# Kernel tuning notes

Measured on AMD Instinct MI355X. Metric: run time of the kernel, lower is better.

## Reference

```python
import jax, jax.numpy as jnp
import numpy as np

N_EVENTS = 16384   # original pixel events
D = 128            # input_size
H = 128            # hidden_size
K = 9              # kernel 3x3 -> patch coords
S = 2048           # number of patch sequences
LMAX = 108         # max sequence length
T = 147456         # total patch events = sum(lengths) = 9 * N_EVENTS


def setup_inputs() -> dict:
    key = jax.random.key(0)
    ks = jax.random.split(key, 8)
    events = jax.random.normal(ks[0], (N_EVENTS, D), jnp.float32)
    pos_id = jax.random.randint(ks[1], (T,), 0, K, dtype=jnp.int32)
    orig_event_idx = jax.random.randint(ks[2], (T,), 0, N_EVENTS, dtype=jnp.int32)
    # alternating 36/108 lengths: 1024*36 + 1024*108 = 147456 = T
    lengths = jnp.where(jnp.arange(S) % 2 == 0, 36, 108).astype(jnp.int32)
    std = float(np.sqrt(2.0 / (D + H)))
    scatter_w = jax.random.normal(ks[3], (K, H, D), jnp.float32) * std
    gather_w = jax.random.normal(ks[4], (K, H, H), jnp.float32) * std
    lstm_std = float(1.0 / np.sqrt(H))
    w_ih = jax.random.uniform(ks[5], (4 * H, H), jnp.float32, -lstm_std, lstm_std)
    w_hh = jax.random.uniform(ks[6], (4 * H, H), jnp.float32, -lstm_std, lstm_std)
    ln_g = jnp.ones((H,), jnp.float32)
    ln_b = jnp.zeros((H,), jnp.float32)
    return dict(events=events, scatter_w=scatter_w, gather_w=gather_w,
                w_ih=w_ih, w_hh=w_hh, ln_g=ln_g, ln_b=ln_b,
                pos_id=pos_id, orig_event_idx=orig_event_idx, lengths=lengths)


def _pos_proj(x, W, pos_id):
    # position-indexed projection: out[t] = W[pos_id[t]] @ x[t]
    # loop over small fixed K=9 with masked accumulate (matches the torch loop)
    out = jnp.zeros((x.shape[0], W.shape[1]), x.dtype)
    for k in range(W.shape[0]):
        out = out + jnp.where((pos_id == k)[:, None], x @ W[k].T, 0.0)
    return out


def reference(events, scatter_w, gather_w, w_ih, w_hh, ln_g, ln_b,
              pos_id, orig_event_idx, lengths):
    # scatter events to patch replicas
    x = events[orig_event_idx]                           # [T, D]
    x = _pos_proj(x, scatter_w, pos_id)                  # [T, H]

    # flat (sequence-major) -> padded [S, LMAX, H]
    seq_offsets = jnp.cumsum(lengths) - lengths          # [S]
    seq_ids = jnp.repeat(jnp.arange(S), lengths, total_repeat_length=T)
    pos_in_seq = jnp.arange(T) - seq_offsets[seq_ids]
    padded = jnp.zeros((S, LMAX, H), x.dtype).at[seq_ids, pos_in_seq].set(x)

    # single-layer bias-free LSTM (pytorch gate order i, f, g, o), zero init.
    # zero-padding after each sequence's valid region leaves valid outputs
    # identical to a PackedSequence LSTM.
    def step(carry, xt):                                 # xt: [S, H]
        h, c = carry
        gates = xt @ w_ih.T + h @ w_hh.T                 # [S, 4H]
        i, f, g, o = jnp.split(gates, 4, axis=-1)
        c = jax.nn.sigmoid(f) * c + jax.nn.sigmoid(i) * jnp.tanh(g)
        h = jax.nn.sigmoid(o) * jnp.tanh(c)
        return (h, c), h

    init = (jnp.zeros((S, H), x.dtype), jnp.zeros((S, H), x.dtype))
    _, hs = jax.lax.scan(step, init, jnp.swapaxes(padded, 0, 1))  # [LMAX, S, H]
    o_flat = jnp.swapaxes(hs, 0, 1)[seq_ids, pos_in_seq]          # [T, H]

    o_flat = _pos_proj(o_flat, gather_w, pos_id)                  # [T, H]

    # gather patch events back to pixel events (scatter-add) + residual + LN
    out = jnp.zeros((N_EVENTS, H), x.dtype).at[orig_event_idx].add(o_flat)
    out = out + events                                   # input_proj is None (D == H)
    mu = jnp.mean(out, axis=-1, keepdims=True)
    var = jnp.var(out, axis=-1, keepdims=True)
    out = (out - mu) * jax.lax.rsqrt(var + 1e-5) * ln_g + ln_b
    return out
```

## Files before the change

### kernel.cpp

```cpp
#include <hip/hip_runtime.h>

#define N_EVENTS 16384
#define DIM 128
#define NK 9
#define NSEQ 2048
#define TT 147456
#define CHUNK 64
#define NCHUNK_MAX (TT/CHUNK + NK)
#define NHBLK 576

typedef __attribute__((ext_vector_type(8))) short bf16x8;
typedef __attribute__((ext_vector_type(4))) float f32x4;
typedef __attribute__((ext_vector_type(4))) int i32x4;

#define OFF_EV     0UL
#define OFF_WC     (OFF_EV   + (size_t)N_EVENTS*DIM*2)
#define OFF_SCAT   (OFF_WC   + (size_t)512*256*2)
#define OFF_GATH   (OFF_SCAT + (size_t)NK*DIM*DIM*2)
#define OFF_XS     (OFF_GATH + (size_t)NK*DIM*DIM*2)
#define OFF_HS     (OFF_XS   + (size_t)TT*DIM*2)
#define OFF_KLIST  (OFF_HS   + (size_t)TT*DIM*2)
#define OFF_ACC    (OFF_KLIST+ (size_t)TT*4)
#define OFF_SEQOFF (OFF_ACC  + (size_t)N_EVENTS*DIM*4)
#define OFF_GROUP  (OFF_SEQOFF + (size_t)NSEQ*4)
#define OFF_MISC   (OFF_GROUP  + (size_t)NSEQ*4)
#define OFF_BH     (OFF_MISC   + 256UL)

__device__ __forceinline__ short f2b(float f) {
    union { float f; unsigned u; } v; v.f = f;
    unsigned r = (v.u + 0x7FFFu + ((v.u >> 16) & 1u)) >> 16;
    return (short)r;
}

__device__ __forceinline__ float fsig(float x) {
    return __builtin_amdgcn_rcpf(1.f + __expf(-x));
}
__device__ __forceinline__ float ftanh(float x) {
    return 1.f - 2.f * __builtin_amdgcn_rcpf(__expf(2.f * x) + 1.f);
}

__global__ void convert_kernel(const float* __restrict__ ev, const float* __restrict__ wih,
                               const float* __restrict__ whh, const float* __restrict__ sw,
                               const float* __restrict__ gw,
                               short* __restrict__ evb, short* __restrict__ wcb,
                               short* __restrict__ swb, short* __restrict__ gwb,
                               float* __restrict__ acc) {
    int idx = blockIdx.x * blockDim.x + threadIdx.x;
    if (idx < N_EVENTS * DIM) { evb[idx] = f2b(ev[idx]); acc[idx] = 0.f; }
    if (idx < 512 * DIM) {
        int j = idx >> 7, d = idx & 127;
        wcb[j * 256 + d]       = f2b(wih[idx]);
        wcb[j * 256 + 128 + d] = f2b(whh[idx]);
    }
    if (idx < NK * DIM * DIM) { swb[idx] = f2b(sw[idx]); gwb[idx] = f2b(gw[idx]); }
}

__global__ void hist_kernel(const int* __restrict__ pos, int* __restrict__ blockhist) {
    __shared__ int h[NK];
    int tid = threadIdx.x;
    if (tid < NK) h[tid] = 0;
    __syncthreads();
    atomicAdd(&h[pos[blockIdx.x * 256 + tid]], 1);
    __syncthreads();
    if (tid < NK) blockhist[blockIdx.x * NK + tid] = h[tid];
}

__global__ void scan_kernel(int* __restrict__ blockhist, int* __restrict__ misc) {
    __shared__ int h[NHBLK * NK];
    int tid = threadIdx.x;
    for (int i = tid; i < NHBLK * NK; i += 256) h[i] = blockhist[i];
    __syncthreads();
    if (tid < NK) {
        int run = 0;
        for (int b = 0; b < NHBLK; b++) {
            int v = h[b * NK + tid];
            h[b * NK + tid] = run;
            run += v;
        }
        misc[tid] = run;
    }
    __syncthreads();
    if (tid == 0) {
        int ko = 0, co = 0;
        for (int k = 0; k < NK; k++) {
            int c = misc[k];
            misc[32 + k] = ko;
            misc[48 + k] = co;
            ko += c;
            co += (c + CHUNK - 1) / CHUNK;
        }
        misc[48 + NK] = co;
    }
    __syncthreads();
    for (int i = tid; i < NHBLK * NK; i += 256) blockhist[i] = h[i];
}

__global__ void setup_kernel(const int* __restrict__ lengths,
                             int* __restrict__ seq_off, int* __restrict__ grouped) {
    __shared__ int lens[NSEQ];
    __shared__ int tsum[256], tlong[256];
    int tid = threadIdx.x;
    for (int i = tid; i < NSEQ; i += 256) lens[i] = lengths[i];
    __syncthreads();
    int base = tid * 8;
    int ls[8]; int s = 0, lc = 0;
    #pragma unroll
    for (int i = 0; i < 8; i++) { ls[i] = lens[base + i]; s += ls[i]; lc += (ls[i] > 64) ? 1 : 0; }
    tsum[tid] = s; tlong[tid] = lc;
    __syncthreads();
    for (int d = 1; d < 256; d <<= 1) {
        int a = (tid >= d) ? tsum[tid - d] : 0;
        int b = (tid >= d) ? tlong[tid - d] : 0;
        __syncthreads();
        tsum[tid] += a; tlong[tid] += b;
        __syncthreads();
    }
    int nlong_total = tlong[255];
    int excl = tsum[tid] - s;
    int excl_long = tlong[tid] - lc;
    int run = 0, runl = 0;
    #pragma unroll
    for (int i = 0; i < 8; i++) {
        int sid = base + i;
        seq_off[sid] = excl + run;
        int longs_before = excl_long + runl;
        if (ls[i] > 64) { grouped[longs_before] = sid; runl++; }
        else            { grouped[nlong_total + (sid - longs_before)] = sid; }
        run += ls[i];
    }
}

__global__ void fill2_kernel(const int* __restrict__ pos, const int* __restrict__ blockhist,
                             const int* __restrict__ misc, int* __restrict__ klist) {
    __shared__ int off[NK];
    int tid = threadIdx.x;
    if (tid < NK) off[tid] = misc[32 + tid] + blockhist[blockIdx.x * NK + tid];
    __syncthreads();
    int t = blockIdx.x * 256 + tid;
    int p = atomicAdd(&off[pos[t]], 1);
    klist[p] = t;
}

__global__ void bucket_gemm(const short* __restrict__ src, const short* __restrict__ wall,
                            const int* __restrict__ klist, const int* __restrict__ misc,
                            const int* __restrict__ orig, short* __restrict__ xs_out,
                            float* __restrict__ acc, int mode) {
    const int* chunkoff = misc + 48;
    int b = blockIdx.x;
    if (b >= chunkoff[NK]) return;
    int k = 0;
    while (k < NK - 1 && chunkoff[k + 1] <= b) k++;
    int lc = b - chunkoff[k];
    int cnt = misc[k];
    int base = misc[32 + k] + lc * CHUNK;
    int nv = min(CHUNK, cnt - lc * CHUNK);

    __shared__ int tok[CHUNK], dst[CHUNK];
    __shared__ short A[CHUNK * 136];
    int tid = threadIdx.x;
    if (tid < CHUNK) {
        int tv = klist[base + ((tid < nv) ? tid : 0)];
        tok[tid] = tv;
        dst[tid] = orig[tv];
    }
    __syncthreads();
    {
        int row = tid >> 2, part = tid & 3;
        int ridx = (mode == 0) ? dst[row] : tok[row];
        const i32x4* s4 = (const i32x4*)(src + (size_t)ridx * DIM + part * 32);
        i32x4* d4 = (i32x4*)(A + row * 136 + part * 32);
        d4[0] = s4[0]; d4[1] = s4[1]; d4[2] = s4[2]; d4[3] = s4[3];
    }
    __syncthreads();
    int wave = tid >> 6, lane = tid & 63, l15 = lane & 15, q = lane >> 4;
    const short* wk = wall + (size_t)k * DIM * DIM;
    bf16x8 Bf[2][4];
    #pragma unroll
    for (int nt = 0; nt < 2; nt++) {
        int h = wave * 32 + nt * 16 + l15;
        #pragma unroll
        for (int kt = 0; kt < 4; kt++)
            Bf[nt][kt] = *(const bf16x8*)(wk + h * DIM + kt * 32 + q * 8);
    }
    f32x4 C[4][2];
    #pragma unroll
    for (int mt = 0; mt < 4; mt++)
        #pragma unroll
        for (int nt = 0; nt < 2; nt++) C[mt][nt] = (f32x4){0.f, 0.f, 0.f, 0.f};
    #pragma unroll
    for (int mt = 0; mt < 4; mt++) {
        bf16x8 Afr[4];
        const short* ar = A + (mt * 16 + l15) * 136 + q * 8;
        Afr[0] = *(const bf16x8*)(ar);
        Afr[1] = *(const bf16x8*)(ar + 32);
        Afr[2] = *(const bf16x8*)(ar + 64);
        Afr[3] = *(const bf16x8*)(ar + 96);
        #pragma unroll
        for (int nt = 0; nt < 2; nt++)
            #pragma unroll
            for (int kt = 0; kt < 4; kt++)
                C[mt][nt] = __builtin_amdgcn_mfma_f32_16x16x32_bf16(Afr[kt], Bf[nt][kt], C[mt][nt], 0, 0, 0);
    }
    if (mode == 0) {
        __syncthreads();
        #pragma unroll
        for (int mt = 0; mt < 4; mt++)
            #pragma unroll
            for (int nt = 0; nt < 2; nt++)
                #pragma unroll
                for (int r = 0; r < 4; r++) {
                    int row = mt * 16 + q * 4 + r;
                    int col = wave * 32 + nt * 16 + l15;
                    A[row * 136 + col] = f2b(C[mt][nt][r]);
                }
        __syncthreads();
        int row = tid >> 2, part = tid & 3;
        if (row < nv) {
            const i32x4* s4 = (const i32x4*)(A + row * 136 + part * 32);
            i32x4* d4 = (i32x4*)(xs_out + (size_t)tok[row] * DIM + part * 32);
            d4[0] = s4[0]; d4[1] = s4[1]; d4[2] = s4[2]; d4[3] = s4[3];
        }
    } else {
        #pragma unroll
        for (int mt = 0; mt < 4; mt++)
            #pragma unroll
            for (int nt = 0; nt < 2; nt++)
                #pragma unroll
                for (int r = 0; r < 4; r++) {
                    int row = mt * 16 + q * 4 + r;
                    if (row < nv) {
                        int col = wave * 32 + nt * 16 + l15;
                        atomicAdd(acc + (size_t)dst[row] * DIM + col, C[mt][nt][r]);
                    }
                }
    }
}

#define MF(a, b, c) __builtin_amdgcn_mfma_f32_16x16x32_bf16(a, b, c, 0, 0, 0)

#define LSTM_STEP(J, PF) { \
    const int i_ = ib8 + (J); \
    f32x4 Cxi = {0.f,0.f,0.f,0.f}, Cxf = {0.f,0.f,0.f,0.f}; \
    f32x4 Cxg = {0.f,0.f,0.f,0.f}, Cxo = {0.f,0.f,0.f,0.f}; \
    Cxi = MF(PF[0], Bf[0][0], Cxi); Cxf = MF(PF[0], Bf[1][0], Cxf); \
    Cxg = MF(PF[0], Bf[2][0], Cxg); Cxo = MF(PF[0], Bf[3][0], Cxo); \
    Cxi = MF(PF[1], Bf[0][1], Cxi); Cxf = MF(PF[1], Bf[1][1], Cxf); \
    Cxg = MF(PF[1], Bf[2][1], Cxg); Cxo = MF(PF[1], Bf[3][1], Cxo); \
    Cxi = MF(PF[2], Bf[0][2], Cxi); Cxf = MF(PF[2], Bf[1][2], Cxf); \
    Cxg = MF(PF[2], Bf[2][2], Cxg); Cxo = MF(PF[2], Bf[3][2], Cxo); \
    Cxi = MF(PF[3], Bf[0][3], Cxi); Cxf = MF(PF[3], Bf[1][3], Cxf); \
    Cxg = MF(PF[3], Bf[2][3], Cxg); Cxo = MF(PF[3], Bf[3][3], Cxo); \
    bf16x8 Hf0, Hf1, Hf2, Hf3; \
    { const short* hp_ = hb + (((J) + 7) & 7) * 1088 + l15 * 136 + ql * 8; \
      Hf0 = *(const bf16x8*)(hp_);      Hf1 = *(const bf16x8*)(hp_ + 32); \
      Hf2 = *(const bf16x8*)(hp_ + 64); Hf3 = *(const bf16x8*)(hp_ + 96); } \
    f32x4 Chi = {0.f,0.f,0.f,0.f}, Chf = {0.f,0.f,0.f,0.f}; \
    f32x4 Chg = {0.f,0.f,0.f,0.f}, Cho = {0.f,0.f,0.f,0.f}; \
    Chi = MF(Hf0, Bf[0][4], Chi); Chf = MF(Hf0, Bf[1][4], Chf); \
    Chg = MF(Hf0, Bf[2][4], Chg); Cho = MF(Hf0, Bf[3][4], Cho); \
    Chi = MF(Hf1, Bf[0][5], Chi); Chf = MF(Hf1, Bf[1][5], Chf); \
    Chg = MF(Hf1, Bf[2][5], Chg); Cho = MF(Hf1, Bf[3][5], Cho); \
    Chi = MF(Hf2, Bf[0][6], Chi); Chf = MF(Hf2, Bf[1][6], Chf); \
    Chg = MF(Hf2, Bf[2][6], Chg); Cho = MF(Hf2, Bf[3][6], Cho); \
    Chi = MF(Hf3, Bf[0][7], Chi); Chf = MF(Hf3, Bf[1][7], Chf); \
    Chg = MF(Hf3, Bf[2][7], Chg); Cho = MF(Hf3, Bf[3][7], Cho); \
    if (l15 < 8) { \
        const short* xp_ = xs + xoff; \
        PF[0] = *(const bf16x8*)(xp_);      PF[1] = *(const bf16x8*)(xp_ + 32); \
        PF[2] = *(const bf16x8*)(xp_ + 64); PF[3] = *(const bf16x8*)(xp_ + 96); \
    } \
    xoff += ((i_ + 4) <= my_len) ? DIM : 0; \
    f32x4 Gi = Cxi + Chi, Gf = Cxf + Chf, Gg = Cxg + Chg, Go = Cxo + Cho; \
    { \
        int src_ = lane & 31; \
        float i2 = __shfl(Gi[2], src_, 64), i3 = __shfl(Gi[3], src_, 64); \
        float f2 = __shfl(Gf[2], src_, 64), f3 = __shfl(Gf[3], src_, 64); \
        float g2 = __shfl(Gg[2], src_, 64), g3 = __shfl(Gg[3], src_, 64); \
        float o2 = __shfl(Go[2], src_, 64), o3 = __shfl(Go[3], src_, 64); \
        float iA = lo ? Gi[0] : i2, iB = lo ? Gi[1] : i3; \
        float fA = lo ? Gf[0] : f2, fB = lo ? Gf[1] : f3; \
        float gA = lo ? Gg[0] : g2, gB = lo ? Gg[1] : g3; \
        float oA = lo ? Go[0] : o2, oB = lo ? Go[1] : o3; \
        if (i_ < lenA) { \
            float si = fsig(iA), sf = fsig(fA), so = fsig(oA); \
            float tg = ftanh(gA); \
            float cn = sf * cA + si * tg; \
            float th = ftanh(cn); \
            cA = cn; \
            hb[(J) * 1088 + rowA * 136 + u] = f2b(so * th); \
        } \
        if (i_ < lenB) { \
            float si = fsig(iB), sf = fsig(fB), so = fsig(oB); \
            float tg = ftanh(gB); \
            float cn = sf * cB + si * tg; \
            float th = ftanh(cn); \
            cB = cn; \
            hb[(J) * 1088 + rowB * 136 + u] = f2b(so * th); \
        } \
    } \
    __syncthreads(); \
}

__global__ __launch_bounds__(512, 2) void lstm_kernel(
        const short* __restrict__ xs, const short* __restrict__ wc,
        short* __restrict__ hstore, const int* __restrict__ seq_off,
        const int* __restrict__ grouped, const int* __restrict__ lengths) {
    __shared__ int s_off[8], s_len[8];
    __shared__ short hchunk[11][8][136];
    int tid = threadIdx.x;
    if (tid < 8) {
        int s = grouped[blockIdx.x * 8 + tid];
        s_off[tid] = seq_off[s];
        s_len[tid] = lengths[s];
    }
    for (int j = tid; j < 11 * 8 * 136; j += 512) ((short*)hchunk)[j] = 0;
    __syncthreads();
    int lane = tid & 63, l15 = lane & 15, ql = lane >> 4;
    int wave = tid >> 6;
    int u = wave * 16 + l15;
    short* hb = (short*)hchunk;
    bf16x8 Bf[4][8];
    #pragma unroll
    for (int g = 0; g < 4; g++) {
        int j = g * 128 + u;
        #pragma unroll
        for (int kt = 0; kt < 8; kt++)
            Bf[g][kt] = *(const bf16x8*)(wc + j * 256 + kt * 32 + ql * 8);
    }
    int maxlen = 0;
    #pragma unroll
    for (int i = 0; i < 8; i++) maxlen = max(maxlen, s_len[i]);
    int my_off = (l15 < 8) ? s_off[l15] : 0;
    int my_len = (l15 < 8) ? s_len[l15] : 1;
    bool lo = (ql < 2);
    int rowA = lo ? (ql * 4 + 0) : ((ql - 2) * 4 + 2);
    int rowB = lo ? (ql * 4 + 1) : ((ql - 2) * 4 + 3);
    int lenA = s_len[rowA], lenB = s_len[rowB];
    float cA = 0.f, cB = 0.f;
    bf16x8 Pf0[4], Pf1[4];
    #pragma unroll
    for (int k = 0; k < 4; k++) { Pf0[k] = (bf16x8){0,0,0,0,0,0,0,0}; Pf1[k] = Pf0[k]; }
    int xoff = my_off * DIM + ql * 8;
    if (l15 < 8) {
        const short* xp = xs + xoff;
        Pf0[0] = *(const bf16x8*)(xp);      Pf0[1] = *(const bf16x8*)(xp + 32);
        Pf0[2] = *(const bf16x8*)(xp + 64); Pf0[3] = *(const bf16x8*)(xp + 96);
    }
    int xoff1 = xoff + ((my_len > 1) ? DIM : 0);
    if (l15 < 8) {
        const short* xp = xs + xoff1;
        Pf1[0] = *(const bf16x8*)(xp);      Pf1[1] = *(const bf16x8*)(xp + 32);
        Pf1[2] = *(const bf16x8*)(xp + 64); Pf1[3] = *(const bf16x8*)(xp + 96);
    }
    xoff = xoff1 + ((my_len > 2) ? DIM : 0);

    int nb8 = (maxlen + 7) >> 3;
    for (int ob = 0; ob < nb8; ob++) {
        int ib8 = ob * 8;
        LSTM_STEP(0, Pf0)
        LSTM_STEP(1, Pf1)
        LSTM_STEP(2, Pf0)
        LSTM_STEP(3, Pf1)
        LSTM_STEP(4, Pf0)
        LSTM_STEP(5, Pf1)
        LSTM_STEP(6, Pf0)
        LSTM_STEP(7, Pf1)
        #pragma unroll
        for (int it = 0; it < 2; it++) {
            int idx = tid + it * 512;
            int st = idx >> 7, s = (idx >> 4) & 7, part = idx & 15;
            int ig = ib8 + st;
            if (ig < s_len[s]) {
                i32x4 v = *(const i32x4*)&hchunk[st][s][part * 8];
                *(i32x4*)(hstore + (size_t)(s_off[s] + ig) * DIM + part * 8) = v;
            }
        }
        __syncthreads();
    }
}

__global__ void ln_kernel(const float* __restrict__ acc, const float* __restrict__ events,
                          const float* __restrict__ g, const float* __restrict__ bta,
                          float* __restrict__ out) {
    int tid = threadIdx.x;
    int wave = tid >> 6, lane = tid & 63;
    int e = blockIdx.x * 4 + wave;
    const float2* a2 = (const float2*)(acc + (size_t)e * DIM);
    const float2* e2 = (const float2*)(events + (size_t)e * DIM);
    float2 av = a2[lane], ev = e2[lane];
    float x0 = av.x + ev.x, x1 = av.y + ev.y;
    float sm = x0 + x1, sq = x0 * x0 + x1 * x1;
    #pragma unroll
    for (int m = 1; m < 64; m <<= 1) {
        sm += __shfl_xor(sm, m, 64);
        sq += __shfl_xor(sq, m, 64);
    }
    float mean = sm * (1.f / DIM);
    float var = sq * (1.f / DIM) - mean * mean;
    float rs = rsqrtf(var + 1e-5f);
    float2 gv = ((const float2*)g)[lane], bv = ((const float2*)bta)[lane];
    float2 ov;
    ov.x = (x0 - mean) * rs * gv.x + bv.x;
    ov.y = (x1 - mean) * rs * gv.y + bv.y;
    ((float2*)(out + (size_t)e * DIM))[lane] = ov;
}

extern "C" void kernel_launch(void* const* d_in, const int* in_sizes, int n_in,
                              void* d_out, int out_size, void* d_ws, size_t ws_size,
                              hipStream_t stream) {
    const float* events = (const float*)d_in[0];
    const float* scat   = (const float*)d_in[1];
    const float* gath   = (const float*)d_in[2];
    const float* wih    = (const float*)d_in[3];
    const float* whh    = (const float*)d_in[4];
    const float* lng    = (const float*)d_in[5];
    const float* lnb    = (const float*)d_in[6];
    const int* posid    = (const int*)d_in[7];
    const int* orig     = (const int*)d_in[8];
    const int* lens     = (const int*)d_in[9];
    char* ws = (char*)d_ws;
    short* evb   = (short*)(ws + OFF_EV);
    short* wcb   = (short*)(ws + OFF_WC);
    short* swb   = (short*)(ws + OFF_SCAT);
    short* gwb   = (short*)(ws + OFF_GATH);
    short* xs    = (short*)(ws + OFF_XS);
    short* hs    = (short*)(ws + OFF_HS);
    int*   klist = (int*)(ws + OFF_KLIST);
    float* acc   = (float*)(ws + OFF_ACC);
    int*   seqo  = (int*)(ws + OFF_SEQOFF);
    int*   grp   = (int*)(ws + OFF_GROUP);
    int*   misc  = (int*)(ws + OFF_MISC);
    int*   bh    = (int*)(ws + OFF_BH);
    float* out   = (float*)d_out;

    convert_kernel<<<8192, 256, 0, stream>>>(events, wih, whh, scat, gath, evb, wcb, swb, gwb, acc);
    hist_kernel<<<NHBLK, 256, 0, stream>>>(posid, bh);
    scan_kernel<<<1, 256, 0, stream>>>(bh, misc);
    setup_kernel<<<1, 256, 0, stream>>>(lens, seqo, grp);
    fill2_kernel<<<NHBLK, 256, 0, stream>>>(posid, bh, misc, klist);
    bucket_gemm<<<NCHUNK_MAX, 256, 0, stream>>>(evb, swb, klist, misc, orig, xs, nullptr, 0);
    lstm_kernel<<<256, 512, 0, stream>>>(xs, wcb, hs, seqo, grp, lens);
    bucket_gemm<<<NCHUNK_MAX, 256, 0, stream>>>(hs, gwb, klist, misc, orig, nullptr, acc, 1);
    ln_kernel<<<4096, 256, 0, stream>>>(acc, events, lng, lnb, out);
}
```

Before: 317.7 us.

## Replace float atomic scatter-add with CSR gather-reduce fused into LayerNorm

Instead of the second bucket GEMM doing float atomicAdds into a per-event accumulator, it now writes bf16 projected rows per token into a buffer. A CSR index (per-event counts, prefix offsets, token lists) is built during the histogram and fill passes, and the LayerNorm kernel gathers and sums each event's rows before normalizing. The scan and setup kernels are merged into one multi-block plan kernel to cut launches. This removes contended global float atomics and the accumulator zeroing, but adds integer atomics, a serial-ish prefix scan, bf16 rounding of the partial outputs and an indirect gather in the final kernel.

```diff
diff --git a/kernel.cpp b/kernel.cpp
--- a/kernel.cpp
+++ b/kernel.cpp
@@ -20,8 +20,11 @@
 #define OFF_XS     (OFF_GATH + (size_t)NK*DIM*DIM*2)
 #define OFF_HS     (OFF_XS   + (size_t)TT*DIM*2)
 #define OFF_KLIST  (OFF_HS   + (size_t)TT*DIM*2)
-#define OFF_ACC    (OFF_KLIST+ (size_t)TT*4)
-#define OFF_SEQOFF (OFF_ACC  + (size_t)N_EVENTS*DIM*4)
+#define OFF_ECNT   (OFF_KLIST+ (size_t)TT*4)
+#define OFF_EOFF   (OFF_ECNT + 16384UL*4)
+#define OFF_ECNT2  (OFF_EOFF + 16392UL*4)
+#define OFF_ELIST  (OFF_ECNT2+ 16384UL*4)
+#define OFF_SEQOFF (OFF_ELIST+ (size_t)TT*4)
 #define OFF_GROUP  (OFF_SEQOFF + (size_t)NSEQ*4)
 #define OFF_MISC   (OFF_GROUP  + (size_t)NSEQ*4)
 #define OFF_BH     (OFF_MISC   + 256UL)
@@ -31,7 +34,9 @@
     unsigned r = (v.u + 0x7FFFu + ((v.u >> 16) & 1u)) >> 16;
     return (short)r;
 }
-
+__device__ __forceinline__ float asf(unsigned u) {
+    union { unsigned u; float f; } v; v.u = u; return v.f;
+}
 __device__ __forceinline__ float fsig(float x) {
     return __builtin_amdgcn_rcpf(1.f + __expf(-x));
 }
@@ -44,94 +49,121 @@
                                const float* __restrict__ gw,
                                short* __restrict__ evb, short* __restrict__ wcb,
                                short* __restrict__ swb, short* __restrict__ gwb,
-                               float* __restrict__ acc) {
+                               int* __restrict__ ecnt, int* __restrict__ ecnt2) {
     int idx = blockIdx.x * blockDim.x + threadIdx.x;
-    if (idx < N_EVENTS * DIM) { evb[idx] = f2b(ev[idx]); acc[idx] = 0.f; }
+    if (idx < N_EVENTS * DIM) evb[idx] = f2b(ev[idx]);
     if (idx < 512 * DIM) {
         int j = idx >> 7, d = idx & 127;
         wcb[j * 256 + d]       = f2b(wih[idx]);
         wcb[j * 256 + 128 + d] = f2b(whh[idx]);
     }
     if (idx < NK * DIM * DIM) { swb[idx] = f2b(sw[idx]); gwb[idx] = f2b(gw[idx]); }
-}
-
-__global__ void hist_kernel(const int* __restrict__ pos, int* __restrict__ blockhist) {
+    if (idx < N_EVENTS) { ecnt[idx] = 0; ecnt2[idx] = 0; }
+}
+
+__global__ void hist_kernel(const int* __restrict__ pos, const int* __restrict__ orig,
+                            int* __restrict__ blockhist, int* __restrict__ ecnt) {
     __shared__ int h[NK];
     int tid = threadIdx.x;
     if (tid < NK) h[tid] = 0;
     __syncthreads();
-    atomicAdd(&h[pos[blockIdx.x * 256 + tid]], 1);
+    int t = blockIdx.x * 256 + tid;
+    atomicAdd(&h[pos[t]], 1);
+    atomicAdd(&ecnt[orig[t]], 1);
     __syncthreads();
     if (tid < NK) blockhist[blockIdx.x * NK + tid] = h[tid];
 }
 
-__global__ void scan_kernel(int* __restrict__ blockhist, int* __restrict__ misc) {
-    __shared__ int h[NHBLK * NK];
-    int tid = threadIdx.x;
-    for (int i = tid; i < NHBLK * NK; i += 256) h[i] = blockhist[i];
-    __syncthreads();
-    if (tid < NK) {
-        int run = 0;
-        for (int b = 0; b < NHBLK; b++) {
-            int v = h[b * NK + tid];
-            h[b * NK + tid] = run;
-            run += v;
-        }
-        misc[tid] = run;
-    }
-    __syncthreads();
-    if (tid == 0) {
-        int ko = 0, co = 0;
-        for (int k = 0; k < NK; k++) {
-            int c = misc[k];
-            misc[32 + k] = ko;
-            misc[48 + k] = co;
-            ko += c;
-            co += (c + CHUNK - 1) / CHUNK;
-        }
-        misc[48 + NK] = co;
-    }
-    __syncthreads();
-    for (int i = tid; i < NHBLK * NK; i += 256) blockhist[i] = h[i];
-}
-
-__global__ void setup_kernel(const int* __restrict__ lengths,
-                             int* __restrict__ seq_off, int* __restrict__ grouped) {
-    __shared__ int lens[NSEQ];
-    __shared__ int tsum[256], tlong[256];
-    int tid = threadIdx.x;
-    for (int i = tid; i < NSEQ; i += 256) lens[i] = lengths[i];
-    __syncthreads();
-    int base = tid * 8;
-    int ls[8]; int s = 0, lc = 0;
-    #pragma unroll
-    for (int i = 0; i < 8; i++) { ls[i] = lens[base + i]; s += ls[i]; lc += (ls[i] > 64) ? 1 : 0; }
-    tsum[tid] = s; tlong[tid] = lc;
-    __syncthreads();
-    for (int d = 1; d < 256; d <<= 1) {
-        int a = (tid >= d) ? tsum[tid - d] : 0;
-        int b = (tid >= d) ? tlong[tid - d] : 0;
-        __syncthreads();
-        tsum[tid] += a; tlong[tid] += b;
-        __syncthreads();
-    }
-    int nlong_total = tlong[255];
-    int excl = tsum[tid] - s;
-    int excl_long = tlong[tid] - lc;
-    int run = 0, runl = 0;
-    #pragma unroll
-    for (int i = 0; i < 8; i++) {
-        int sid = base + i;
-        seq_off[sid] = excl + run;
-        int longs_before = excl_long + runl;
-        if (ls[i] > 64) { grouped[longs_before] = sid; runl++; }
-        else            { grouped[nlong_total + (sid - longs_before)] = sid; }
-        run += ls[i];
-    }
-}
-
-__global__ void fill2_kernel(const int* __restrict__ pos, const int* __restrict__ blockhist,
-                             const int* __restrict__ misc, int* __restrict__ klist) {
+__global__ void plan_kernel(int* __restrict__ blockhist, int* __restrict__ misc,
+                            const int* __restrict__ lengths, int* __restrict__ seq_off,
+                            int* __restrict__ grouped,
+                            const int* __restrict__ ecnt, int* __restrict__ eoff) {
+    int tid = threadIdx.x;
+    if (blockIdx.x == 0) {
+        __shared__ int h[NHBLK * NK];
+        for (int i = tid; i < NHBLK * NK; i += 256) h[i] = blockhist[i];
+        __syncthreads();
+        if (tid < NK) {
+            int run = 0;
+            for (int b = 0; b < NHBLK; b++) {
+                int v = h[b * NK + tid];
+                h[b * NK + tid] = run;
+                run += v;
+            }
+            misc[tid] = run;
+        }
+        __syncthreads();
+        if (tid == 0) {
+            int ko = 0, co = 0;
+            for (int k = 0; k < NK; k++) {
+                int c = misc[k];
+                misc[32 + k] = ko;
+                misc[48 + k] = co;
+                ko += c;
+                co += (c + CHUNK - 1) / CHUNK;
+            }
+            misc[48 + NK] = co;
+        }
+        __syncthreads();
+        for (int i = tid; i < NHBLK * NK; i += 256) blockhist[i] = h[i];
+    } else if (blockIdx.x == 1) {
+        __shared__ int lens[NSEQ];
+        __shared__ int tsum[256], tlong[256];
+        for (int i = tid; i < NSEQ; i += 256) lens[i] = lengths[i];
+        __syncthreads();
+        int base = tid * 8;
+        int ls[8]; int s = 0, lc = 0;
+        #pragma unroll
+        for (int i = 0; i < 8; i++) { ls[i] = lens[base + i]; s += ls[i]; lc += (ls[i] > 64) ? 1 : 0; }
+        tsum[tid] = s; tlong[tid] = lc;
+        __syncthreads();
+        for (int d = 1; d < 256; d <<= 1) {
+            int a = (tid >= d) ? tsum[tid - d] : 0;
+            int b = (tid >= d) ? tlong[tid - d] : 0;
+            __syncthreads();
+            tsum[tid] += a; tlong[tid] += b;
+            __syncthreads();
+        }
+        int nlong_total = tlong[255];
+        int excl = tsum[tid] - s;
+        int excl_long = tlong[tid] - lc;
+        int run = 0, runl = 0;
+        #pragma unroll
+        for (int i = 0; i < 8; i++) {
+            int sid = base + i;
+            seq_off[sid] = excl + run;
+            int lb = excl_long + runl;
+            if (ls[i] > 64) { grouped[lb] = sid; runl++; }
+            else            { grouped[nlong_total + (sid - lb)] = sid; }
+            run += ls[i];
+        }
+    } else {
+        __shared__ int part[256];
+        int base = tid * 64;
+        int s = 0;
+        for (int j = 0; j < 64; j++) s += ecnt[base + j];
+        part[tid] = s;
+        __syncthreads();
+        for (int d = 1; d < 256; d <<= 1) {
+            int a = (tid >= d) ? part[tid - d] : 0;
+            __syncthreads();
+            part[tid] += a;
+            __syncthreads();
+        }
+        int run = part[tid] - s;
+        for (int j = 0; j < 64; j++) {
+            eoff[base + j] = run;
+            run += ecnt[base + j];
+        }
+        if (tid == 255) eoff[N_EVENTS] = run;
+    }
+}
+
+__global__ void fill_kernel(const int* __restrict__ pos, const int* __restrict__ orig,
+                            const int* __restrict__ blockhist, const int* __restrict__ misc,
+                            int* __restrict__ klist,
+                            const int* __restrict__ eoff, int* __restrict__ ecnt2,
+                            int* __restrict__ elist) {
     __shared__ int off[NK];
     int tid = threadIdx.x;
     if (tid < NK) off[tid] = misc[32 + tid] + blockhist[blockIdx.x * NK + tid];
@@ -139,12 +171,15 @@
     int t = blockIdx.x * 256 + tid;
     int p = atomicAdd(&off[pos[t]], 1);
     klist[p] = t;
+    int o = orig[t];
+    int p2 = atomicAdd(&ecnt2[o], 1);
+    elist[eoff[o] + p2] = t;
 }
 
 __global__ void bucket_gemm(const short* __restrict__ src, const short* __restrict__ wall,
                             const int* __restrict__ klist, const int* __restrict__ misc,
-                            const int* __restrict__ orig, short* __restrict__ xs_out,
-                            float* __restrict__ acc, int mode) {
+                            const int* __restrict__ orig, short* __restrict__ rows_out,
+                            int mode) {
     const int* chunkoff = misc + 48;
     int b = blockIdx.x;
     if (b >= chunkoff[NK]) return;
@@ -155,19 +190,18 @@
     int base = misc[32 + k] + lc * CHUNK;
     int nv = min(CHUNK, cnt - lc * CHUNK);
 
-    __shared__ int tok[CHUNK], dst[CHUNK];
+    __shared__ int tok[CHUNK], ridx[CHUNK];
     __shared__ short A[CHUNK * 136];
     int tid = threadIdx.x;
     if (tid < CHUNK) {
         int tv = klist[base + ((tid < nv) ? tid : 0)];
         tok[tid] = tv;
-        dst[tid] = orig[tv];
+        ridx[tid] = (mode == 0) ? orig[tv] : tv;
     }
     __syncthreads();
     {
         int row = tid >> 2, part = tid & 3;
-        int ridx = (mode == 0) ? dst[row] : tok[row];
-        const i32x4* s4 = (const i32x4*)(src + (size_t)ridx * DIM + part * 32);
+        const i32x4* s4 = (const i32x4*)(src + (size_t)ridx[row] * DIM + part * 32);
         i32x4* d4 = (i32x4*)(A + row * 136 + part * 32);
         d4[0] = s4[0]; d4[1] = s4[1]; d4[2] = s4[2]; d4[3] = s4[3];
     }
@@ -201,38 +235,25 @@
             for (int kt = 0; kt < 4; kt++)
                 C[mt][nt] = __builtin_amdgcn_mfma_f32_16x16x32_bf16(Afr[kt], Bf[nt][kt], C[mt][nt], 0, 0, 0);
     }
-    if (mode == 0) {
-        __syncthreads();
-        #pragma unroll
-        for (int mt = 0; mt < 4; mt++)
+    __syncthreads();
+    #pragma unroll
+    for (int mt = 0; mt < 4; mt++)
+        #pragma unroll
+        for (int nt = 0; nt < 2; nt++)
             #pragma unroll
-            for (int nt = 0; nt < 2; nt++)
-                #pragma unroll
-                for (int r = 0; r < 4; r++) {
-                    int row = mt * 16 + q * 4 + r;
-                    int col = wave * 32 + nt * 16 + l15;
-                    A[row * 136 + col] = f2b(C[mt][nt][r]);
-                }
-        __syncthreads();
+            for (int r = 0; r < 4; r++) {
+                int row = mt * 16 + q * 4 + r;
+                int col = wave * 32 + nt * 16 + l15;
+                A[row * 136 + col] = f2b(C[mt][nt][r]);
+            }
+    __syncthreads();
+    {
         int row = tid >> 2, part = tid & 3;
         if (row < nv) {
             const i32x4* s4 = (const i32x4*)(A + row * 136 + part * 32);
-            i32x4* d4 = (i32x4*)(xs_out + (size_t)tok[row] * DIM + part * 32);
+            i32x4* d4 = (i32x4*)(rows_out + (size_t)tok[row] * DIM + part * 32);
             d4[0] = s4[0]; d4[1] = s4[1]; d4[2] = s4[2]; d4[3] = s4[3];
         }
-    } else {
-        #pragma unroll
-        for (int mt = 0; mt < 4; mt++)
-            #pragma unroll
-            for (int nt = 0; nt < 2; nt++)
-                #pragma unroll
-                for (int r = 0; r < 4; r++) {
-                    int row = mt * 16 + q * 4 + r;
-                    if (row < nv) {
-                        int col = wave * 32 + nt * 16 + l15;
-                        atomicAdd(acc + (size_t)dst[row] * DIM + col, C[mt][nt][r]);
-                    }
-                }
     }
 }
 
@@ -379,16 +400,24 @@
     }
 }
 
-__global__ void ln_kernel(const float* __restrict__ acc, const float* __restrict__ events,
+__global__ void gather_ln(const short* __restrict__ of, const int* __restrict__ eoff,
+                          const int* __restrict__ elist, const float* __restrict__ ev,
                           const float* __restrict__ g, const float* __restrict__ bta,
                           float* __restrict__ out) {
     int tid = threadIdx.x;
     int wave = tid >> 6, lane = tid & 63;
     int e = blockIdx.x * 4 + wave;
-    const float2* a2 = (const float2*)(acc + (size_t)e * DIM);
-    const float2* e2 = (const float2*)(events + (size_t)e * DIM);
-    float2 av = a2[lane], ev = e2[lane];
-    float x0 = av.x + ev.x, x1 = av.y + ev.y;
+    int s0 = eoff[e], s1 = eoff[e + 1];
+    float x0 = 0.f, x1 = 0.f;
+    for (int j = s0; j < s1; j++) {
+        int t = elist[j];
+        unsigned v = *(const unsigned*)(of + (size_t)t * DIM + lane * 2);
+        x0 += asf(v << 16);
+        x1 += asf(v & 0xffff0000u);
+    }
+    const float2* e2 = (const float2*)(ev + (size_t)e * DIM);
+    float2 evv = e2[lane];
+    x0 += evv.x; x1 += evv.y;
     float sm = x0 + x1, sq = x0 * x0 + x1 * x1;
     #pragma unroll
     for (int m = 1; m < 64; m <<= 1) {
@@ -426,20 +455,23 @@
     short* xs    = (short*)(ws + OFF_XS);
     short* hs    = (short*)(ws + OFF_HS);
     int*   klist = (int*)(ws + OFF_KLIST);
-    float* acc   = (float*)(ws + OFF_ACC);
+    int*   ecnt  = (int*)(ws + OFF_ECNT);
+    int*   eoff  = (int*)(ws + OFF_EOFF);
+    int*   ecnt2 = (int*)(ws + OFF_ECNT2);
+    int*   elist = (int*)(ws + OFF_ELIST);
     int*   seqo  = (int*)(ws + OFF_SEQOFF);
     int*   grp   = (int*)(ws + OFF_GROUP);
     int*   misc  = (int*)(ws + OFF_MISC);
     int*   bh    = (int*)(ws + OFF_BH);
     float* out   = (float*)d_out;
 
-    convert_kernel<<<8192, 256, 0, stream>>>(events, wih, whh, scat, gath, evb, wcb, swb, gwb, acc);
-    hist_kernel<<<NHBLK, 256, 0, stream>>>(posid, bh);
-    scan_kernel<<<1, 256, 0, stream>>>(bh, misc);
-    setup_kernel<<<1, 256, 0, stream>>>(lens, seqo, grp);
-    fill2_kernel<<<NHBLK, 256, 0, stream>>>(posid, bh, misc, klist);
-    bucket_gemm<<<NCHUNK_MAX, 256, 0, stream>>>(evb, swb, klist, misc, orig, xs, nullptr, 0);
+    convert_kernel<<<8192, 256, 0, stream>>>(events, wih, whh, scat, gath,
+                                             evb, wcb, swb, gwb, ecnt, ecnt2);
+    hist_kernel<<<NHBLK, 256, 0, stream>>>(posid, orig, bh, ecnt);
+    plan_kernel<<<3, 256, 0, stream>>>(bh, misc, lens, seqo, grp, ecnt, eoff);
+    fill_kernel<<<NHBLK, 256, 0, stream>>>(posid, orig, bh, misc, klist, eoff, ecnt2, elist);
+    bucket_gemm<<<NCHUNK_MAX, 256, 0, stream>>>(evb, swb, klist, misc, orig, xs, 0);
     lstm_kernel<<<256, 512, 0, stream>>>(xs, wcb, hs, seqo, grp, lens);
-    bucket_gemm<<<NCHUNK_MAX, 256, 0, stream>>>(hs, gwb, klist, misc, orig, nullptr, acc, 1);
-    ln_kernel<<<4096, 256, 0, stream>>>(acc, events, lng, lnb, out);
-}
+    bucket_gemm<<<NCHUNK_MAX, 256, 0, stream>>>(hs, gwb, klist, misc, orig, xs, 1);
+    gather_ln<<<4096, 256, 0, stream>>>(xs, eoff, elist, events, lng, lnb, out);
+}
```

Measured after the change: 300.3 us. 5.5% less time.
